# Optimization experiments

Hardware: AMD Instinct MI355X
Metric: run time of the kernel (lower is better)

## Reference

```python
import jax, jax.numpy as jnp
import numpy as np

B, S, D, H = 2, 2048, 1024, 16
HD = D // H  # head_dim = 64


def setup_inputs() -> dict:
    key = jax.random.key(0)
    ks = jax.random.split(key, 10)
    scale = 0.02
    return {
        "features": jax.random.normal(ks[0], (B, S, D), dtype=jnp.float32),
        "attention_mask": jnp.zeros((B, 1, S, S), dtype=jnp.float32),
        "wq": jax.random.normal(ks[1], (D, D), dtype=jnp.float32) * scale,
        "bq": jnp.zeros((D,), dtype=jnp.float32),
        "wk": jax.random.normal(ks[2], (D, D), dtype=jnp.float32) * scale,
        "bk": jnp.zeros((D,), dtype=jnp.float32),
        "wv": jax.random.normal(ks[3], (D, D), dtype=jnp.float32) * scale,
        "bv": jnp.zeros((D,), dtype=jnp.float32),
        "wo": jax.random.normal(ks[4], (D, D), dtype=jnp.float32) * scale,
        "bo": jnp.zeros((D,), dtype=jnp.float32),
    }


def _split_heads(x):
    # [B,S,D] -> [B,H,S,HD]
    return x.reshape(B, S, H, HD).transpose(0, 2, 1, 3)


def reference(features, attention_mask, wq, bq, wk, bk, wv, bv, wo, bo):
    scaling = HD ** -0.5
    # torch Linear: y = x @ W.T + b; Bart scales q by head_dim**-0.5
    q = _split_heads((features @ wq.T + bq) * scaling)
    k = _split_heads(features @ wk.T + bk)
    v = _split_heads(features @ wv.T + bv)
    scores = jnp.einsum("bhqd,bhkd->bhqk", q, k) + attention_mask
    attn = jax.nn.softmax(scores, axis=-1)
    ctx = jnp.einsum("bhqk,bhkd->bhqd", attn, v)
    ctx = ctx.transpose(0, 2, 1, 3).reshape(B, S, D)
    gated = ctx @ wo.T + bo
    out = features * gated
    return (out, gated)
```

## Files before the change

kernel.cpp:

```cpp
#include <hip/hip_runtime.h>
#include <math.h>

#define Bc 2
#define Sc 2048
#define Dc 1024
#define Hc 16
#define HDc 64
#define NROWS 4096

typedef __attribute__((ext_vector_type(8))) _Float16 f16x8;
typedef __attribute__((ext_vector_type(4))) _Float16 f16x4;
typedef __attribute__((ext_vector_type(2))) __fp16 fp16v2;
typedef __attribute__((ext_vector_type(4))) float f32x4;

__global__ __launch_bounds__(256)
void cvt5(const float* __restrict__ f,  const float* __restrict__ wq,
          const float* __restrict__ wk, const float* __restrict__ wv,
          const float* __restrict__ wo_,
          _Float16* __restrict__ fh, _Float16* __restrict__ wh3,
          _Float16* __restrict__ woh)
{
  int blk = blockIdx.x;
  const float* src; _Float16* hi; int base;
  if (blk < 4096)      { src = f;   hi = fh;            base = blk; }
  else if (blk < 5120) { src = wq;  hi = wh3;           base = blk - 4096; }
  else if (blk < 6144) { src = wk;  hi = wh3 + 1048576; base = blk - 5120; }
  else if (blk < 7168) { src = wv;  hi = wh3 + 2097152; base = blk - 6144; }
  else                 { src = wo_; hi = woh;           base = blk - 7168; }
  int i = base * 256 + threadIdx.x;
  float4 v = reinterpret_cast<const float4*>(src)[i];
  f16x4 h;
  h[0] = (_Float16)v.x; h[1] = (_Float16)v.y;
  h[2] = (_Float16)v.z; h[3] = (_Float16)v.w;
  reinterpret_cast<f16x4*>(hi)[i] = h;
}

__global__ __launch_bounds__(256, 4)
void gemm_qkv(const _Float16* __restrict__ Ah, const _Float16* __restrict__ Wh,
              const float* __restrict__ bq, const float* __restrict__ bk,
              const float* __restrict__ bv,
              _Float16* __restrict__ qb, _Float16* __restrict__ kb,
              _Float16* __restrict__ vtb)
{
  __shared__ _Float16 Ash[128][40];
  __shared__ _Float16 Wsh[128][40];

  const int tid  = threadIdx.x;
  const int lane = tid & 63, wid = tid >> 6;
  const int l15  = lane & 15, l4 = lane >> 4;
  const int wr   = wid >> 1, wc = wid & 1;
  const int arow0 = blockIdx.x * 128;
  const int wrow0 = blockIdx.y * 128;

  f32x4 acc[4][4];
#pragma unroll
  for (int m = 0; m < 4; ++m)
#pragma unroll
    for (int n = 0; n < 4; ++n) acc[m][n] = f32x4{0.f, 0.f, 0.f, 0.f};

  for (int k0 = 0; k0 < Dc; k0 += 32) {
    __syncthreads();
#pragma unroll
    for (int p = 0; p < 2; ++p) {
      int e = tid + 256 * p;
      int r = e >> 2, c8 = (e & 3) * 8;
      *reinterpret_cast<uint4*>(&Ash[r][c8]) =
          *reinterpret_cast<const uint4*>(Ah + (size_t)(arow0 + r) * Dc + k0 + c8);
      *reinterpret_cast<uint4*>(&Wsh[r][c8]) =
          *reinterpret_cast<const uint4*>(Wh + (size_t)(wrow0 + r) * Dc + k0 + c8);
    }
    __syncthreads();

    f16x8 bh[4];
#pragma unroll
    for (int n = 0; n < 4; ++n)
      bh[n] = *reinterpret_cast<const f16x8*>(&Wsh[wc * 64 + n * 16 + l15][l4 * 8]);
#pragma unroll
    for (int m = 0; m < 4; ++m) {
      f16x8 ah = *reinterpret_cast<const f16x8*>(&Ash[wr * 64 + m * 16 + l15][l4 * 8]);
#pragma unroll
      for (int n = 0; n < 4; ++n)
        acc[m][n] = __builtin_amdgcn_mfma_f32_16x16x32_f16(ah, bh[n], acc[m][n], 0, 0, 0);
    }
  }

#pragma unroll
  for (int m = 0; m < 4; ++m) {
#pragma unroll
    for (int n = 0; n < 4; ++n) {
      int cbase = wrow0 + wc * 64 + n * 16;
      int seg = cbase >> 10;
      int o = (cbase & 1023) + l15;
      int h = o >> 6, hd = o & 63;
      const float* bias = (seg == 0) ? bq : ((seg == 1) ? bk : bv);
      float bval = bias[o];
      float alpha = (seg == 0) ? 0.125f : 1.0f;
      int r0 = arow0 + wr * 64 + m * 16 + l4 * 4;
      int b = r0 >> 11, s0 = r0 & (Sc - 1);
      if (seg == 2) {
        f16x4 pk;
#pragma unroll
        for (int reg = 0; reg < 4; ++reg)
          pk[reg] = (_Float16)((acc[m][n][reg] + bval) * alpha);
        *reinterpret_cast<f16x4*>(
            &vtb[(((size_t)b * Hc + h) * HDc + hd) * Sc + s0]) = pk;
      } else {
        _Float16* dst = (seg == 0) ? qb : kb;
#pragma unroll
        for (int reg = 0; reg < 4; ++reg) {
          float val = (acc[m][n][reg] + bval) * alpha;
          dst[(((size_t)b * Hc + h) * Sc + (s0 + reg)) * HDc + hd] = (_Float16)val;
        }
      }
    }
  }
}

__global__ __launch_bounds__(256, 4)
void gemm_wo(const _Float16* __restrict__ Ah, const _Float16* __restrict__ Wh,
             const float* __restrict__ bias,
             float* __restrict__ out0, float* __restrict__ out1,
             const float* __restrict__ feats)
{
  __shared__ _Float16 Ash[64][40];
  __shared__ _Float16 Wsh[128][40];

  const int tid  = threadIdx.x;
  const int lane = tid & 63, wid = tid >> 6;
  const int l15  = lane & 15, l4 = lane >> 4;
  const int wr   = wid >> 1, wc = wid & 1;
  const int arow0 = blockIdx.x * 64;
  const int wrow0 = blockIdx.y * 128;

  f32x4 acc[2][4];
#pragma unroll
  for (int m = 0; m < 2; ++m)
#pragma unroll
    for (int n = 0; n < 4; ++n) acc[m][n] = f32x4{0.f, 0.f, 0.f, 0.f};

  for (int k0 = 0; k0 < Dc; k0 += 32) {
    __syncthreads();
    {
      int r = tid >> 2, c8 = (tid & 3) * 8;
      *reinterpret_cast<uint4*>(&Ash[r][c8]) =
          *reinterpret_cast<const uint4*>(Ah + (size_t)(arow0 + r) * Dc + k0 + c8);
    }
#pragma unroll
    for (int p = 0; p < 2; ++p) {
      int e = tid + 256 * p;
      int r = e >> 2, c8 = (e & 3) * 8;
      *reinterpret_cast<uint4*>(&Wsh[r][c8]) =
          *reinterpret_cast<const uint4*>(Wh + (size_t)(wrow0 + r) * Dc + k0 + c8);
    }
    __syncthreads();

    f16x8 bh[4];
#pragma unroll
    for (int n = 0; n < 4; ++n)
      bh[n] = *reinterpret_cast<const f16x8*>(&Wsh[wc * 64 + n * 16 + l15][l4 * 8]);
#pragma unroll
    for (int m = 0; m < 2; ++m) {
      f16x8 ah = *reinterpret_cast<const f16x8*>(&Ash[wr * 32 + m * 16 + l15][l4 * 8]);
#pragma unroll
      for (int n = 0; n < 4; ++n)
        acc[m][n] = __builtin_amdgcn_mfma_f32_16x16x32_f16(ah, bh[n], acc[m][n], 0, 0, 0);
    }
  }

#pragma unroll
  for (int m = 0; m < 2; ++m) {
#pragma unroll
    for (int n = 0; n < 4; ++n) {
      int c = wrow0 + wc * 64 + n * 16 + l15;
      float bval = bias[c];
#pragma unroll
      for (int reg = 0; reg < 4; ++reg) {
        int r = arow0 + wr * 32 + m * 16 + l4 * 4 + reg;
        float val = acc[m][n][reg] + bval;
        out1[(size_t)r * Dc + c] = val;
        out0[(size_t)r * Dc + c] = feats[(size_t)r * Dc + c] * val;
      }
    }
  }
}

#define QB 128
#define KB 64
#define NT (Sc / KB)

__global__ __launch_bounds__(512, 4)
void attn_mfma(const _Float16* __restrict__ q,
               const _Float16* __restrict__ k,
               const _Float16* __restrict__ vt,
               const float* __restrict__ mask,
               _Float16* __restrict__ ctxh)
{
  __shared__ _Float16 Ks[2][KB * 64];
  __shared__ _Float16 Vs[2][HDc * 64];
  __shared__ _Float16 Ps[8][16][72];

  const int tid  = threadIdx.x;
  const int lane = tid & 63;
  const int wave = tid >> 6;
  const int l15  = lane & 15;
  const int l4   = lane >> 4;

  const int nqb  = Sc / QB;
  const int head = blockIdx.x / nqb;
  const int q0   = (blockIdx.x % nqb) * QB;
  const int b    = head / Hc;
  const int h    = head % Hc;

  const _Float16* qbase  = q  + ((size_t)head * Sc + q0 + wave * 16) * HDc;
  const _Float16* kbase  = k  + (size_t)head * Sc * HDc;
  const _Float16* vtbase = vt + (size_t)head * HDc * Sc;
  const float*    mbase  = mask + ((size_t)b * Sc + q0 + wave * 16) * Sc;
  const float*    mlane  = mbase + (size_t)l15 * Sc + l4 * 4;

  const int srow  = tid >> 3;
  const int scol  = tid & 7;
  const int sofs  = srow * 64 + (scol ^ (srow & 7)) * 8;

  const int c0 = ((l4)     ^ (l15 & 7)) * 8;
  const int c1 = ((l4 + 4) ^ (l15 & 7)) * 8;

  f16x8 qf[2];
#pragma unroll
  for (int f = 0; f < 2; ++f)
    qf[f] = *reinterpret_cast<const f16x8*>(
        qbase + (size_t)l15 * HDc + l4 * 8 + 32 * f);

  f16x8 ones;
#pragma unroll
  for (int i = 0; i < 8; ++i) ones[i] = (_Float16)1.0f;

  f32x4 O[4];
#pragma unroll
  for (int dt = 0; dt < 4; ++dt) O[dt] = f32x4{0.f, 0.f, 0.f, 0.f};
  float m_q = -3e38f;
  float l_r[4];
#pragma unroll
  for (int r = 0; r < 4; ++r) l_r[r] = 0.f;

  *reinterpret_cast<uint4*>(&Ks[0][sofs]) =
      *reinterpret_cast<const uint4*>(kbase + (size_t)srow * HDc + scol * 8);
  *reinterpret_cast<uint4*>(&Vs[0][sofs]) =
      *reinterpret_cast<const uint4*>(vtbase + (size_t)srow * Sc + scol * 8);
  float4 mpf[4];
#pragma unroll
  for (int nt = 0; nt < 4; ++nt)
    mpf[nt] = *reinterpret_cast<const float4*>(mlane + 16 * nt);

  for (int kt = 0; kt < NT; ++kt) {
    const int k0 = kt * KB;
    const int cur = kt & 1, nxt = cur ^ 1;
    __syncthreads();

    uint4 kr, vr;
    const bool pf = (kt + 1) < NT;
    if (pf) {
      const int k1 = k0 + KB;
      kr = *reinterpret_cast<const uint4*>(kbase + (size_t)(k1 + srow) * HDc + scol * 8);
      vr = *reinterpret_cast<const uint4*>(vtbase + (size_t)srow * Sc + k1 + scol * 8);
    }

    f32x4 s[4];
    __builtin_amdgcn_s_setprio(1);
#pragma unroll
    for (int nt = 0; nt < 4; ++nt) {
      const int krow = (16 * nt + l15) * 64;
      f32x4 acc = f32x4{0.f, 0.f, 0.f, 0.f};
      acc = __builtin_amdgcn_mfma_f32_16x16x32_f16(
          *reinterpret_cast<const f16x8*>(&Ks[cur][krow + c0]), qf[0], acc, 0, 0, 0);
      acc = __builtin_amdgcn_mfma_f32_16x16x32_f16(
          *reinterpret_cast<const f16x8*>(&Ks[cur][krow + c1]), qf[1], acc, 0, 0, 0);
      s[nt] = acc;
    }
    __builtin_amdgcn_s_setprio(0);

#pragma unroll
    for (int nt = 0; nt < 4; ++nt) {
      s[nt][0] += mpf[nt].x; s[nt][1] += mpf[nt].y;
      s[nt][2] += mpf[nt].z; s[nt][3] += mpf[nt].w;
    }
    if (pf) {
#pragma unroll
      for (int nt = 0; nt < 4; ++nt)
        mpf[nt] = *reinterpret_cast<const float4*>(mlane + (k0 + KB) + 16 * nt);
    }

    float lm = s[0][0];
#pragma unroll
    for (int nt = 0; nt < 4; ++nt)
#pragma unroll
      for (int reg = 0; reg < 4; ++reg) lm = fmaxf(lm, s[nt][reg]);

    if (!__all(lm - m_q <= 8.0f)) {
      float vm = fmaxf(lm, __shfl_xor(lm, 16));
      vm = fmaxf(vm, __shfl_xor(vm, 32));
      float mn = fmaxf(m_q, vm);
      float cc = __expf(m_q - mn);
      m_q = mn;
#pragma unroll
      for (int reg = 0; reg < 4; ++reg) {
        float ccq = __shfl(cc, l4 * 4 + reg);
        l_r[reg] *= ccq;
#pragma unroll
        for (int dt = 0; dt < 4; ++dt) O[dt][reg] *= ccq;
      }
    }

#pragma unroll
    for (int nt = 0; nt < 4; ++nt) {
      float p0 = __expf(s[nt][0] - m_q);
      float p1 = __expf(s[nt][1] - m_q);
      float p2 = __expf(s[nt][2] - m_q);
      float p3 = __expf(s[nt][3] - m_q);
      union { uint2 u; fp16v2 h[2]; } pk;
      pk.h[0] = __builtin_amdgcn_cvt_pkrtz(p0, p1);
      pk.h[1] = __builtin_amdgcn_cvt_pkrtz(p2, p3);
      *reinterpret_cast<uint2*>(&Ps[wave][l15][16 * nt + l4 * 4]) = pk.u;
    }

    asm volatile("" ::: "memory");

    f16x8 pa0 = *reinterpret_cast<const f16x8*>(&Ps[wave][l15][l4 * 8]);
    f16x8 pa1 = *reinterpret_cast<const f16x8*>(&Ps[wave][l15][l4 * 8 + 32]);

    __builtin_amdgcn_s_setprio(1);
    f32x4 lacc = f32x4{0.f, 0.f, 0.f, 0.f};
    lacc = __builtin_amdgcn_mfma_f32_16x16x32_f16(pa0, ones, lacc, 0, 0, 0);
    lacc = __builtin_amdgcn_mfma_f32_16x16x32_f16(pa1, ones, lacc, 0, 0, 0);

#pragma unroll
    for (int dt = 0; dt < 4; ++dt) {
      const int vrow = (16 * dt + l15) * 64;
      O[dt] = __builtin_amdgcn_mfma_f32_16x16x32_f16(
          pa0, *reinterpret_cast<const f16x8*>(&Vs[cur][vrow + c0]), O[dt], 0, 0, 0);
      O[dt] = __builtin_amdgcn_mfma_f32_16x16x32_f16(
          pa1, *reinterpret_cast<const f16x8*>(&Vs[cur][vrow + c1]), O[dt], 0, 0, 0);
    }
    __builtin_amdgcn_s_setprio(0);

#pragma unroll
    for (int reg = 0; reg < 4; ++reg) l_r[reg] += lacc[reg];

    if (pf) {
      *reinterpret_cast<uint4*>(&Ks[nxt][sofs]) = kr;
      *reinterpret_cast<uint4*>(&Vs[nxt][sofs]) = vr;
    }
  }

  float inv[4];
#pragma unroll
  for (int reg = 0; reg < 4; ++reg) inv[reg] = 1.0f / l_r[reg];
#pragma unroll
  for (int dt = 0; dt < 4; ++dt)
#pragma unroll
    for (int reg = 0; reg < 4; ++reg) {
      int row = q0 + wave * 16 + l4 * 4 + reg;
      size_t addr = ((size_t)b * Sc + row) * Dc + h * HDc + l15 + 16 * dt;
      ctxh[addr] = (_Float16)(O[dt][reg] * inv[reg]);
    }
}

extern "C" void kernel_launch(void* const* d_in, const int* in_sizes, int n_in,
                              void* d_out, int out_size, void* d_ws, size_t ws_size,
                              hipStream_t stream) {
  const float* feats = (const float*)d_in[0];
  const float* mask  = (const float*)d_in[1];
  const float* wq    = (const float*)d_in[2];
  const float* bq    = (const float*)d_in[3];
  const float* wk    = (const float*)d_in[4];
  const float* bk    = (const float*)d_in[5];
  const float* wv    = (const float*)d_in[6];
  const float* bv    = (const float*)d_in[7];
  const float* wo    = (const float*)d_in[8];
  const float* bo    = (const float*)d_in[9];

  char* ws = (char*)d_ws;
  const size_t MB = (size_t)1 << 20;
  _Float16* fh   = (_Float16*)(ws);
  _Float16* wh3  = (_Float16*)(ws + 8  * MB);
  _Float16* woh  = (_Float16*)(ws + 14 * MB);
  _Float16* qb   = (_Float16*)(ws + 16 * MB);
  _Float16* kb   = (_Float16*)(ws + 24 * MB);
  _Float16* vtb  = (_Float16*)(ws + 32 * MB);
  _Float16* ctxh = (_Float16*)(ws + 40 * MB);

  float* out   = (float*)d_out;
  float* gated = out + 4194304;

  cvt5<<<8192, 256, 0, stream>>>(feats, wq, wk, wv, wo, fh, wh3, woh);

  gemm_qkv<<<dim3(NROWS / 128, 3072 / 128), 256, 0, stream>>>(
      fh, wh3, bq, bk, bv, qb, kb, vtb);

  attn_mfma<<<Bc * Hc * (Sc / QB), 512, 0, stream>>>(qb, kb, vtb, mask, ctxh);

  gemm_wo<<<dim3(NROWS / 64, Dc / 128), 256, 0, stream>>>(
      ctxh, woh, bo, out, gated, feats);
}
```

Measured before the change: 160.0 us.

## Switch attention to 32x32x16 MFMA with register-resident P via permlane32 swap

Rewrites the flash-attention inner loop to use 32x32x16 MFMA tiles, with each of four waves owning 32 query rows instead of eight waves owning 16. The probability tile is now rearranged in registers with v_permlane32_swap instead of a round trip through shared memory, so the P staging buffer goes away. The row-sum accumulator is folded into a 16-wide MFMA accumulator that is rescaled together with O. Block size drops to 256 threads with a different launch-bounds occupancy hint, which trades thread parallelism for larger per-wave tiles, more registers, and less LDS traffic.

```diff
diff --git a/kernel.cpp b/kernel.cpp
--- a/kernel.cpp
+++ b/kernel.cpp
@@ -12,6 +12,7 @@
 typedef __attribute__((ext_vector_type(4))) _Float16 f16x4;
 typedef __attribute__((ext_vector_type(2))) __fp16 fp16v2;
 typedef __attribute__((ext_vector_type(4))) float f32x4;
+typedef __attribute__((ext_vector_type(16))) float f32x16;
 
 __global__ __launch_bounds__(256)
 void cvt5(const float* __restrict__ f,  const float* __restrict__ wq,
@@ -188,7 +189,7 @@
 #define KB 64
 #define NT (Sc / KB)
 
-__global__ __launch_bounds__(512, 4)
+__global__ __launch_bounds__(256, 2)
 void attn_mfma(const _Float16* __restrict__ q,
                const _Float16* __restrict__ k,
                const _Float16* __restrict__ vt,
@@ -197,13 +198,12 @@
 {
   __shared__ _Float16 Ks[2][KB * 64];
   __shared__ _Float16 Vs[2][HDc * 64];
-  __shared__ _Float16 Ps[8][16][72];
 
   const int tid  = threadIdx.x;
   const int lane = tid & 63;
-  const int wave = tid >> 6;
-  const int l15  = lane & 15;
-  const int l4   = lane >> 4;
+  const int wq   = tid >> 6;
+  const int l31  = lane & 31;
+  const int hi   = lane >> 5;
 
   const int nqb  = Sc / QB;
   const int head = blockIdx.x / nqb;
@@ -211,157 +211,162 @@
   const int b    = head / Hc;
   const int h    = head % Hc;
 
-  const _Float16* qbase  = q  + ((size_t)head * Sc + q0 + wave * 16) * HDc;
   const _Float16* kbase  = k  + (size_t)head * Sc * HDc;
   const _Float16* vtbase = vt + (size_t)head * HDc * Sc;
-  const float*    mbase  = mask + ((size_t)b * Sc + q0 + wave * 16) * Sc;
-  const float*    mlane  = mbase + (size_t)l15 * Sc + l4 * 4;
-
-  const int srow  = tid >> 3;
-  const int scol  = tid & 7;
-  const int sofs  = srow * 64 + (scol ^ (srow & 7)) * 8;
-
-  const int c0 = ((l4)     ^ (l15 & 7)) * 8;
-  const int c1 = ((l4 + 4) ^ (l15 & 7)) * 8;
-
-  f16x8 qf[2];
-#pragma unroll
-  for (int f = 0; f < 2; ++f)
-    qf[f] = *reinterpret_cast<const f16x8*>(
-        qbase + (size_t)l15 * HDc + l4 * 8 + 32 * f);
+  const _Float16* qbase  = q  + ((size_t)head * Sc + q0 + wq * 32 + l31) * HDc;
+  const float*    ml     = mask + ((size_t)b * Sc + q0 + wq * 32 + l31) * Sc + 4 * hi;
+
+  const int r0s = tid >> 3, cs = tid & 7;
+  const int r1s = r0s + 32;
+  const int so0 = r0s * 64 + ((cs ^ (r0s & 7)) * 8);
+  const int so1 = r1s * 64 + ((cs ^ (r1s & 7)) * 8);
+
+  f16x8 qf[4];
+#pragma unroll
+  for (int c = 0; c < 4; ++c)
+    qf[c] = *reinterpret_cast<const f16x8*>(qbase + hi * 8 + 16 * c);
 
   f16x8 ones;
 #pragma unroll
   for (int i = 0; i < 8; ++i) ones[i] = (_Float16)1.0f;
 
-  f32x4 O[4];
-#pragma unroll
-  for (int dt = 0; dt < 4; ++dt) O[dt] = f32x4{0.f, 0.f, 0.f, 0.f};
+  f32x16 O0, O1, lacc;
+#pragma unroll
+  for (int i = 0; i < 16; ++i) { O0[i] = 0.f; O1[i] = 0.f; lacc[i] = 0.f; }
   float m_q = -3e38f;
-  float l_r[4];
-#pragma unroll
-  for (int r = 0; r < 4; ++r) l_r[r] = 0.f;
-
-  *reinterpret_cast<uint4*>(&Ks[0][sofs]) =
-      *reinterpret_cast<const uint4*>(kbase + (size_t)srow * HDc + scol * 8);
-  *reinterpret_cast<uint4*>(&Vs[0][sofs]) =
-      *reinterpret_cast<const uint4*>(vtbase + (size_t)srow * Sc + scol * 8);
-  float4 mpf[4];
-#pragma unroll
-  for (int nt = 0; nt < 4; ++nt)
-    mpf[nt] = *reinterpret_cast<const float4*>(mlane + 16 * nt);
+
+  *reinterpret_cast<uint4*>(&Ks[0][so0]) =
+      *reinterpret_cast<const uint4*>(kbase + (size_t)r0s * HDc + cs * 8);
+  *reinterpret_cast<uint4*>(&Ks[0][so1]) =
+      *reinterpret_cast<const uint4*>(kbase + (size_t)r1s * HDc + cs * 8);
+  *reinterpret_cast<uint4*>(&Vs[0][so0]) =
+      *reinterpret_cast<const uint4*>(vtbase + (size_t)r0s * Sc + cs * 8);
+  *reinterpret_cast<uint4*>(&Vs[0][so1]) =
+      *reinterpret_cast<const uint4*>(vtbase + (size_t)r1s * Sc + cs * 8);
+  float4 mpf[8];
+#pragma unroll
+  for (int t2 = 0; t2 < 2; ++t2)
+#pragma unroll
+    for (int j = 0; j < 4; ++j)
+      mpf[t2 * 4 + j] = *reinterpret_cast<const float4*>(ml + 32 * t2 + 8 * j);
 
   for (int kt = 0; kt < NT; ++kt) {
     const int k0 = kt * KB;
     const int cur = kt & 1, nxt = cur ^ 1;
     __syncthreads();
 
-    uint4 kr, vr;
+    uint4 kr0, kr1, vr0, vr1;
     const bool pf = (kt + 1) < NT;
     if (pf) {
       const int k1 = k0 + KB;
-      kr = *reinterpret_cast<const uint4*>(kbase + (size_t)(k1 + srow) * HDc + scol * 8);
-      vr = *reinterpret_cast<const uint4*>(vtbase + (size_t)srow * Sc + k1 + scol * 8);
-    }
-
-    f32x4 s[4];
+      kr0 = *reinterpret_cast<const uint4*>(kbase + (size_t)(k1 + r0s) * HDc + cs * 8);
+      kr1 = *reinterpret_cast<const uint4*>(kbase + (size_t)(k1 + r1s) * HDc + cs * 8);
+      vr0 = *reinterpret_cast<const uint4*>(vtbase + (size_t)r0s * Sc + k1 + cs * 8);
+      vr1 = *reinterpret_cast<const uint4*>(vtbase + (size_t)r1s * Sc + k1 + cs * 8);
+    }
+
+    f32x16 s[2];
     __builtin_amdgcn_s_setprio(1);
 #pragma unroll
-    for (int nt = 0; nt < 4; ++nt) {
-      const int krow = (16 * nt + l15) * 64;
-      f32x4 acc = f32x4{0.f, 0.f, 0.f, 0.f};
-      acc = __builtin_amdgcn_mfma_f32_16x16x32_f16(
-          *reinterpret_cast<const f16x8*>(&Ks[cur][krow + c0]), qf[0], acc, 0, 0, 0);
-      acc = __builtin_amdgcn_mfma_f32_16x16x32_f16(
-          *reinterpret_cast<const f16x8*>(&Ks[cur][krow + c1]), qf[1], acc, 0, 0, 0);
-      s[nt] = acc;
+    for (int t2 = 0; t2 < 2; ++t2) {
+      f32x16 acc;
+#pragma unroll
+      for (int i = 0; i < 16; ++i) acc[i] = 0.f;
+      const int krow = t2 * 32 + l31;
+#pragma unroll
+      for (int c = 0; c < 4; ++c) {
+        const int ofs = krow * 64 + (((2 * c + hi) ^ (krow & 7)) * 8);
+        acc = __builtin_amdgcn_mfma_f32_32x32x16_f16(
+            *reinterpret_cast<const f16x8*>(&Ks[cur][ofs]), qf[c], acc, 0, 0, 0);
+      }
+      s[t2] = acc;
     }
     __builtin_amdgcn_s_setprio(0);
 
 #pragma unroll
-    for (int nt = 0; nt < 4; ++nt) {
-      s[nt][0] += mpf[nt].x; s[nt][1] += mpf[nt].y;
-      s[nt][2] += mpf[nt].z; s[nt][3] += mpf[nt].w;
-    }
+    for (int t2 = 0; t2 < 2; ++t2)
+#pragma unroll
+      for (int j = 0; j < 4; ++j) {
+        float4 mv = mpf[t2 * 4 + j];
+        s[t2][4 * j + 0] += mv.x; s[t2][4 * j + 1] += mv.y;
+        s[t2][4 * j + 2] += mv.z; s[t2][4 * j + 3] += mv.w;
+      }
     if (pf) {
 #pragma unroll
-      for (int nt = 0; nt < 4; ++nt)
-        mpf[nt] = *reinterpret_cast<const float4*>(mlane + (k0 + KB) + 16 * nt);
+      for (int t2 = 0; t2 < 2; ++t2)
+#pragma unroll
+        for (int j = 0; j < 4; ++j)
+          mpf[t2 * 4 + j] = *reinterpret_cast<const float4*>(
+              ml + (k0 + KB) + 32 * t2 + 8 * j);
     }
 
     float lm = s[0][0];
 #pragma unroll
-    for (int nt = 0; nt < 4; ++nt)
-#pragma unroll
-      for (int reg = 0; reg < 4; ++reg) lm = fmaxf(lm, s[nt][reg]);
+    for (int t2 = 0; t2 < 2; ++t2)
+#pragma unroll
+      for (int i = 0; i < 16; ++i) lm = fmaxf(lm, s[t2][i]);
 
     if (!__all(lm - m_q <= 8.0f)) {
-      float vm = fmaxf(lm, __shfl_xor(lm, 16));
-      vm = fmaxf(vm, __shfl_xor(vm, 32));
+      float vm = fmaxf(lm, __shfl_xor(lm, 32));
       float mn = fmaxf(m_q, vm);
       float cc = __expf(m_q - mn);
       m_q = mn;
 #pragma unroll
-      for (int reg = 0; reg < 4; ++reg) {
-        float ccq = __shfl(cc, l4 * 4 + reg);
-        l_r[reg] *= ccq;
-#pragma unroll
-        for (int dt = 0; dt < 4; ++dt) O[dt][reg] *= ccq;
+      for (int reg = 0; reg < 16; ++reg) {
+        int q_r = (reg & 3) + 8 * (reg >> 2) + 4 * hi;
+        float ccr = __shfl(cc, q_r);
+        O0[reg] *= ccr; O1[reg] *= ccr; lacc[reg] *= ccr;
       }
     }
 
-#pragma unroll
-    for (int nt = 0; nt < 4; ++nt) {
-      float p0 = __expf(s[nt][0] - m_q);
-      float p1 = __expf(s[nt][1] - m_q);
-      float p2 = __expf(s[nt][2] - m_q);
-      float p3 = __expf(s[nt][3] - m_q);
-      union { uint2 u; fp16v2 h[2]; } pk;
-      pk.h[0] = __builtin_amdgcn_cvt_pkrtz(p0, p1);
-      pk.h[1] = __builtin_amdgcn_cvt_pkrtz(p2, p3);
-      *reinterpret_cast<uint2*>(&Ps[wave][l15][16 * nt + l4 * 4]) = pk.u;
-    }
-
-    asm volatile("" ::: "memory");
-
-    f16x8 pa0 = *reinterpret_cast<const f16x8*>(&Ps[wave][l15][l4 * 8]);
-    f16x8 pa1 = *reinterpret_cast<const f16x8*>(&Ps[wave][l15][l4 * 8 + 32]);
-
     __builtin_amdgcn_s_setprio(1);
-    f32x4 lacc = f32x4{0.f, 0.f, 0.f, 0.f};
-    lacc = __builtin_amdgcn_mfma_f32_16x16x32_f16(pa0, ones, lacc, 0, 0, 0);
-    lacc = __builtin_amdgcn_mfma_f32_16x16x32_f16(pa1, ones, lacc, 0, 0, 0);
-
-#pragma unroll
-    for (int dt = 0; dt < 4; ++dt) {
-      const int vrow = (16 * dt + l15) * 64;
-      O[dt] = __builtin_amdgcn_mfma_f32_16x16x32_f16(
-          pa0, *reinterpret_cast<const f16x8*>(&Vs[cur][vrow + c0]), O[dt], 0, 0, 0);
-      O[dt] = __builtin_amdgcn_mfma_f32_16x16x32_f16(
-          pa1, *reinterpret_cast<const f16x8*>(&Vs[cur][vrow + c1]), O[dt], 0, 0, 0);
+#pragma unroll
+    for (int c = 0; c < 4; ++c) {
+      const int t2 = c >> 1, rb = (c & 1) * 8;
+      float p0 = __expf(s[t2][rb + 0] - m_q);
+      float p1 = __expf(s[t2][rb + 1] - m_q);
+      float p2 = __expf(s[t2][rb + 2] - m_q);
+      float p3 = __expf(s[t2][rb + 3] - m_q);
+      float p4 = __expf(s[t2][rb + 4] - m_q);
+      float p5 = __expf(s[t2][rb + 5] - m_q);
+      float p6 = __expf(s[t2][rb + 6] - m_q);
+      float p7 = __expf(s[t2][rb + 7] - m_q);
+      union { fp16v2 h; unsigned int u; } w0, w1, w2, w3;
+      w0.h = __builtin_amdgcn_cvt_pkrtz(p0, p1);
+      w1.h = __builtin_amdgcn_cvt_pkrtz(p2, p3);
+      w2.h = __builtin_amdgcn_cvt_pkrtz(p4, p5);
+      w3.h = __builtin_amdgcn_cvt_pkrtz(p6, p7);
+      unsigned int u0 = w0.u, u1 = w1.u, u2 = w2.u, u3 = w3.u;
+      asm("v_permlane32_swap_b32 %0, %1" : "+v"(u0), "+v"(u2));
+      asm("v_permlane32_swap_b32 %0, %1" : "+v"(u1), "+v"(u3));
+      union { unsigned int u[4]; f16x8 f; } pa;
+      pa.u[0] = u0; pa.u[1] = u1; pa.u[2] = u2; pa.u[3] = u3;
+
+      lacc = __builtin_amdgcn_mfma_f32_32x32x16_f16(pa.f, ones, lacc, 0, 0, 0);
+      const int vofs = l31 * 64 + (((2 * c + hi) ^ (l31 & 7)) * 8);
+      O0 = __builtin_amdgcn_mfma_f32_32x32x16_f16(
+          pa.f, *reinterpret_cast<const f16x8*>(&Vs[cur][vofs]), O0, 0, 0, 0);
+      O1 = __builtin_amdgcn_mfma_f32_32x32x16_f16(
+          pa.f, *reinterpret_cast<const f16x8*>(&Vs[cur][vofs + 32 * 64]), O1, 0, 0, 0);
     }
     __builtin_amdgcn_s_setprio(0);
 
-#pragma unroll
-    for (int reg = 0; reg < 4; ++reg) l_r[reg] += lacc[reg];
-
     if (pf) {
-      *reinterpret_cast<uint4*>(&Ks[nxt][sofs]) = kr;
-      *reinterpret_cast<uint4*>(&Vs[nxt][sofs]) = vr;
-    }
-  }
-
-  float inv[4];
-#pragma unroll
-  for (int reg = 0; reg < 4; ++reg) inv[reg] = 1.0f / l_r[reg];
-#pragma unroll
-  for (int dt = 0; dt < 4; ++dt)
-#pragma unroll
-    for (int reg = 0; reg < 4; ++reg) {
-      int row = q0 + wave * 16 + l4 * 4 + reg;
-      size_t addr = ((size_t)b * Sc + row) * Dc + h * HDc + l15 + 16 * dt;
-      ctxh[addr] = (_Float16)(O[dt][reg] * inv[reg]);
-    }
+      *reinterpret_cast<uint4*>(&Ks[nxt][so0]) = kr0;
+      *reinterpret_cast<uint4*>(&Ks[nxt][so1]) = kr1;
+      *reinterpret_cast<uint4*>(&Vs[nxt][so0]) = vr0;
+      *reinterpret_cast<uint4*>(&Vs[nxt][so1]) = vr1;
+    }
+  }
+
+#pragma unroll
+  for (int reg = 0; reg < 16; ++reg) {
+    int q_r = (reg & 3) + 8 * (reg >> 2) + 4 * hi;
+    float inv = 1.0f / lacc[reg];
+    size_t rowbase = ((size_t)b * Sc + (q0 + wq * 32 + q_r)) * Dc + h * HDc;
+    ctxh[rowbase + l31]      = (_Float16)(O0[reg] * inv);
+    ctxh[rowbase + 32 + l31] = (_Float16)(O1[reg] * inv);
+  }
 }
 
 extern "C" void kernel_launch(void* const* d_in, const int* in_sizes, int n_in,
@@ -396,7 +401,7 @@
   gemm_qkv<<<dim3(NROWS / 128, 3072 / 128), 256, 0, stream>>>(
       fh, wh3, bq, bk, bv, qb, kb, vtb);
 
-  attn_mfma<<<Bc * Hc * (Sc / QB), 512, 0, stream>>>(qb, kb, vtb, mask, ctxh);
+  attn_mfma<<<Bc * Hc * (Sc / QB), 256, 0, stream>>>(qb, kb, vtb, mask, ctxh);
 
   gemm_wo<<<dim3(NROWS / 64, Dc / 128), 256, 0, stream>>>(
       ctxh, woh, bo, out, gated, feats);
```

After: 159.1 us. No clear change (-0.6%).
